# Optimization experiments

Hardware: AMD Instinct MI355X
Metric: run time of the kernel (lower is better)

## Reference

```python
import jax, jax.numpy as jnp
import numpy as np
from jax import lax


def leaky(x):
    return jax.nn.leaky_relu(x, 0.01)


def masked_softmax(vec, mask, eps=1e-6):
    # softmax over entries where mask>0; zero elsewhere (stable via masked max)
    mask = mask.astype(vec.dtype)
    mx = jnp.max(jnp.where(mask > 0, vec, -jnp.inf), axis=1, keepdims=True)
    mx = jnp.where(jnp.isfinite(mx), mx, 0.0)
    e = jnp.exp(vec - mx) * mask
    return e / (e.sum(axis=1, keepdims=True) + eps)


def gru_dir(x, w_ih, w_hh, b_ih, b_hh, reverse):
    # PyTorch GRU cell math, one direction. x: [T, in]
    gi_all = x @ w_ih.T + b_ih  # [T, 3*GH], input gates precomputed
    def step(h, gi):
        gh = h @ w_hh.T + b_hh
        i_r, i_z, i_n = jnp.split(gi, 3)
        h_r, h_z, h_n = jnp.split(gh, 3)
        r = jax.nn.sigmoid(i_r + h_r)
        z = jax.nn.sigmoid(i_z + h_z)
        n = jnp.tanh(i_n + r * h_n)
        h2 = (1.0 - z) * n + z * h
        return h2, h2
    h0 = jnp.zeros((w_hh.shape[1],), x.dtype)
    _, ys = lax.scan(step, h0, gi_all, reverse=reverse)
    return ys  # [T, GH]


def setup_inputs():
    key = jax.random.key(0)
    ks = jax.random.split(key, 30)
    W, P, R, H = 128, 4096, 8192, 1024
    GH = H // 2
    s = 0.05
    def nrm(k, shp, sc):
        return jax.random.normal(k, shp, jnp.float32) * sc
    return {
        "word_feat": nrm(ks[0], (W, H), 1.0),
        "phrase_feat": nrm(ks[1], (P, H), 1.0),
        "rel_feat": nrm(ks[2], (R, H), 1.0),
        "w_ih_f": nrm(ks[3], (3 * GH, H), s), "w_hh_f": nrm(ks[4], (3 * GH, GH), s),
        "b_ih_f": nrm(ks[5], (3 * GH,), s), "b_hh_f": nrm(ks[6], (3 * GH,), s),
        "w_ih_b": nrm(ks[7], (3 * GH, H), s), "w_hh_b": nrm(ks[8], (3 * GH, GH), s),
        "b_ih_b": nrm(ks[9], (3 * GH,), s), "b_hh_b": nrm(ks[10], (3 * GH,), s),
        "w2p_w_W": nrm(ks[11], (H, H), s), "w2p_w_b": nrm(ks[12], (H,), s),
        "w2p_p_W": nrm(ks[13], (H, H), s), "w2p_p_b": nrm(ks[14], (H,), s),
        "w2p_t_W": nrm(ks[15], (H, H), s), "w2p_t_b": nrm(ks[16], (H,), s),
        "rel_W": nrm(ks[17], (H, 3 * H), s), "rel_b": nrm(ks[18], (H,), s),
        "att1_W": nrm(ks[19], (H, 4 * H), s), "att1_b": nrm(ks[20], (H,), s),
        "att2_W": nrm(ks[21], (1, H), s), "att2_b": nrm(ks[22], (1,), s),
        "r2p_t_W": nrm(ks[23], (H, H), s), "r2p_t_b": nrm(ks[24], (H,), s),
        "rel_conn_mat": jax.random.randint(ks[25], (2, R), 0, P),
        "word_to_graph_conn": jax.random.randint(ks[26], (P, W), 0, 2),
    }


def reference(word_feat, phrase_feat, rel_feat, w_ih_f, w_hh_f, b_ih_f, b_hh_f,
              w_ih_b, w_hh_b, b_ih_b, b_hh_b, w2p_w_W, w2p_w_b, w2p_p_W, w2p_p_b,
              w2p_t_W, w2p_t_b, rel_W, rel_b, att1_W, att1_b, att2_W, att2_b,
              r2p_t_W, r2p_t_b, rel_conn_mat, word_to_graph_conn):
    H = word_feat.shape[1]
    # bidirectional GRU over the word sequence
    lf = jnp.concatenate([
        gru_dir(word_feat, w_ih_f, w_hh_f, b_ih_f, b_hh_f, False),
        gru_dir(word_feat, w_ih_b, w_hh_b, b_ih_b, b_hh_b, True),
    ], axis=1)  # [T, H]
    ctx = jnp.concatenate([lf[0], lf[-1]])[None, :]  # [1, 2H]
    # word -> phrase attention
    a = (leaky(phrase_feat @ w2p_p_W.T + w2p_p_b)
         @ leaky(word_feat @ w2p_w_W.T + w2p_w_b).T) / jnp.sqrt(jnp.float32(H))
    a = masked_softmax(a, word_to_graph_conn)
    upd = phrase_feat + (a @ word_feat) @ w2p_t_W.T + w2p_t_b  # [P, H]
    # phrase -> rel
    sub, obj = rel_conn_mat[0], rel_conn_mat[1]
    Rn = sub.shape[0]
    Pn = upd.shape[0]
    urel = jnp.concatenate([upd[sub], upd[obj], rel_feat], 1) @ rel_W.T + rel_b  # [R, H]
    # rel -> phrase with sparse connectivity (each rel touches subject+object)
    ar = jnp.arange(Rn)
    mask = jnp.zeros((Pn, Rn), upd.dtype).at[sub, ar].set(1.0).at[obj, ar].set(1.0)
    ix = jnp.concatenate([sub, obj])
    iy = jnp.concatenate([ar, ar])
    fuse = jnp.concatenate(
        [upd[ix], urel[iy], jnp.broadcast_to(ctx, (ix.shape[0], ctx.shape[1]))], 1)  # [2R, 4H]
    s = (leaky(fuse @ att1_W.T + att1_b) @ att2_W.T + att2_b)[:, 0]
    att = jnp.zeros((Pn, Rn), upd.dtype).at[ix, iy].set(s)
    att = masked_softmax(att, mask)
    out_phrase = upd + (att @ urel) @ r2p_t_W.T + r2p_t_b
    return (word_feat, out_phrase, urel)
```

## Files before the change

kernel.cpp:

```cpp
#include <hip/hip_runtime.h>

#define DEV __device__ __forceinline__

typedef short s16x8 __attribute__((ext_vector_type(8)));
typedef float f32x4 __attribute__((ext_vector_type(4)));
typedef __fp16 fp16x8 __attribute__((ext_vector_type(8)));
typedef unsigned short u16;
typedef unsigned long long u64;

constexpr int Wn = 128;
constexpr int Pn = 4096;
constexpr int Rn = 8192;
constexpr int Hn = 1024;

DEV float b2f(u16 u) { union { unsigned i; float f; } x; x.i = (unsigned)u << 16; return x.f; }
DEV u16 f2b(float f) {
  union { float f; unsigned i; } x; x.f = f;
  unsigned r = x.i + 0x7FFF + ((x.i >> 16) & 1);
  return (u16)(r >> 16);
}
DEV u16 f2h(float x) { __fp16 h = (__fp16)x; u16 r; __builtin_memcpy(&r, &h, 2); return r; }
DEV float leaky(float x) { return x >= 0.f ? x : 0.01f * x; }

DEV void load_lds16(const void* g, void* l) {
  __builtin_amdgcn_global_load_lds(
      (const __attribute__((address_space(1))) void*)g,
      (__attribute__((address_space(3))) void*)l, 16, 0, 0);
}

DEV float wred_sum(float v) {
  #pragma unroll
  for (int m = 1; m < 64; m <<= 1) v += __shfl_xor(v, m, 64);
  return v;
}
DEV float wred_max(float v) {
  #pragma unroll
  for (int m = 1; m < 64; m <<= 1) v = fmaxf(v, __shfl_xor(v, m, 64));
  return v;
}

__global__ __launch_bounds__(256) void k_cvt(
    const float* __restrict__ src, int sld, u16* __restrict__ dst)
{
  int g = blockIdx.x * 256 + threadIdx.x;
  int row = g >> 7, c = (g & 127) * 8;
  const float* s = src + (size_t)row * sld + c;
  float4 a = *(const float4*)s;
  float4 b = *(const float4*)(s + 4);
  ushort4 lo = {f2b(a.x), f2b(a.y), f2b(a.z), f2b(a.w)};
  ushort4 hi = {f2b(b.x), f2b(b.y), f2b(b.z), f2b(b.w)};
  *(ushort4*)(dst + (size_t)row * 1024 + c) = lo;
  *(ushort4*)(dst + (size_t)row * 1024 + c + 4) = hi;
}

template<bool OUTF32, bool ACT, bool BIAS, bool RES, bool DUAL>
DEV void gemm_tile(char* sm,
    const u16* __restrict__ A, int lda, const u16* __restrict__ B, int ldb,
    void* Cp, int ldc, const float* __restrict__ bias,
    const float* res, int ldr, u16* C16, float alpha, int K, int m0, int n0)
{
  char* As = sm;
  char* Bs = sm + 16384;
  const int tid = threadIdx.x;
  const int lane = tid & 63, w = tid >> 6;
  const int wr = (w >> 1) * 64, wc = (w & 1) * 64;
  const int r_lo = lane & 15, kq = lane >> 4;

  __syncthreads();

  f32x4 acc[4][4];
  #pragma unroll
  for (int i = 0; i < 4; ++i)
    #pragma unroll
    for (int j = 0; j < 4; ++j) acc[i][j] = (f32x4){0.f, 0.f, 0.f, 0.f};

  for (int kt = 0; kt < K; kt += 64) {
    if (kt) __syncthreads();
    #pragma unroll
    for (int i = 0; i < 4; ++i) {
      int f = i * 4096 + tid * 16;
      int row = f >> 7, colb = f & 127;
      int scol = colb ^ ((row & 7) << 4);
      load_lds16((const char*)(A + (size_t)(m0 + row) * lda + kt) + scol,
                 As + i * 4096 + w * 1024);
    }
    #pragma unroll
    for (int i = 0; i < 4; ++i) {
      int f = i * 4096 + tid * 16;
      int row = f >> 7, colb = f & 127;
      int scol = colb ^ ((row & 7) << 4);
      load_lds16((const char*)(B + (size_t)(n0 + row) * ldb + kt) + scol,
                 Bs + i * 4096 + w * 1024);
    }
    __syncthreads();
    #pragma unroll
    for (int ks = 0; ks < 2; ++ks) {
      s16x8 af[4], bfr[4];
      const int kb = ks * 64 + kq * 16;
      #pragma unroll
      for (int mi = 0; mi < 4; ++mi) {
        int row = wr + mi * 16 + r_lo;
        af[mi] = *(const s16x8*)(As + row * 128 + (kb ^ ((row & 7) << 4)));
      }
      #pragma unroll
      for (int ni = 0; ni < 4; ++ni) {
        int row = wc + ni * 16 + r_lo;
        bfr[ni] = *(const s16x8*)(Bs + row * 128 + (kb ^ ((row & 7) << 4)));
      }
      #pragma unroll
      for (int mi = 0; mi < 4; ++mi)
        #pragma unroll
        for (int ni = 0; ni < 4; ++ni)
          acc[mi][ni] = __builtin_amdgcn_mfma_f32_16x16x32_bf16(af[mi], bfr[ni], acc[mi][ni], 0, 0, 0);
    }
  }
  #pragma unroll
  for (int mi = 0; mi < 4; ++mi)
    #pragma unroll
    for (int ni = 0; ni < 4; ++ni)
      #pragma unroll
      for (int j = 0; j < 4; ++j) {
        int r = m0 + wr + mi * 16 + kq * 4 + j;
        int c = n0 + wc + ni * 16 + r_lo;
        float v = acc[mi][ni][j] * alpha;
        if (BIAS) v += bias[c];
        if (RES)  v += res[(size_t)r * ldr + c];
        if (ACT)  v = leaky(v);
        if (OUTF32) ((float*)Cp)[(size_t)r * ldc + c] = v;
        else        ((u16*)Cp)[(size_t)r * ldc + c] = f2b(v);
        if (DUAL)   C16[(size_t)r * ldc + c] = f2b(v);
      }
}

template<bool OUTF32, bool ACT, bool BIAS, bool RES, bool DUAL>
__global__ __launch_bounds__(256) void k_gemm_bt(
    const u16* __restrict__ A, int lda, const u16* __restrict__ B, int ldb,
    void* Cp, int ldc, const float* __restrict__ bias,
    const float* res, int ldr, u16* C16, float alpha, int K)
{
  __shared__ __align__(16) char sm[32768];
  gemm_tile<OUTF32, ACT, BIAS, RES, DUAL>(sm, A, lda, B, ldb, Cp, ldc, bias,
      res, ldr, C16, alpha, K, blockIdx.y * 128, blockIdx.x * 128);
}

__global__ __launch_bounds__(256) void k_rf3(
    const u16* __restrict__ G, const u16* __restrict__ relU,
    const u16* __restrict__ W3s, const float* __restrict__ rel_b,
    float* __restrict__ out_urel)
{
  __shared__ __align__(16) char sm[32768];
  int half = blockIdx.y >> 5;
  gemm_tile<true, false, true, false, false>(sm,
      half ? relU : G, Hn, W3s, Hn,
      out_urel + (size_t)half * 4096 * Hn, Hn, rel_b, nullptr, 0, nullptr,
      1.f, Hn, (blockIdx.y & 31) * 128, blockIdx.x * 128);
}

__global__ __launch_bounds__(256) void k_gemm_rel(
    const u16* __restrict__ upd16, const int* __restrict__ rcm,
    const u16* __restrict__ W1, const u16* __restrict__ W2,
    float* __restrict__ out_urel)
{
  __shared__ __align__(16) char sm[32768];
  __shared__ int ridx[2][128];
  char* As = sm;
  char* Bs = sm + 16384;
  const int tid = threadIdx.x;
  const int lane = tid & 63, w = tid >> 6;
  const int hh = blockIdx.y >> 5;
  const int m0 = (blockIdx.y & 31) * 128, n0 = blockIdx.x * 128;
  const int wr = (w >> 1) * 64, wc = (w & 1) * 64;
  const int r_lo = lane & 15, kq = lane >> 4;
  const int* sub = rcm + hh * 4096;
  const int* obj = rcm + Rn + hh * 4096;
  float* C = out_urel + (size_t)hh * 4096 * Hn;

  if (tid < 128) ridx[0][tid] = sub[m0 + tid];
  else ridx[1][tid - 128] = obj[m0 + tid - 128];
  __syncthreads();

  f32x4 acc[4][4];
  #pragma unroll
  for (int i = 0; i < 4; ++i)
    #pragma unroll
    for (int j = 0; j < 4; ++j) acc[i][j] = (f32x4){0.f, 0.f, 0.f, 0.f};

  for (int kt = 0; kt < 2048; kt += 64) {
    const int half = kt >> 10;
    const int kk = kt & 1023;
    const u16* Wm = half ? W2 : W1;
    __syncthreads();
    #pragma unroll
    for (int i = 0; i < 4; ++i) {
      int f = i * 4096 + tid * 16;
      int row = f >> 7, colb = f & 127;
      int scol = colb ^ ((row & 7) << 4);
      load_lds16((const char*)(upd16 + (size_t)ridx[half][row] * 1024 + kk) + scol,
                 As + i * 4096 + w * 1024);
    }
    #pragma unroll
    for (int i = 0; i < 4; ++i) {
      int f = i * 4096 + tid * 16;
      int row = f >> 7, colb = f & 127;
      int scol = colb ^ ((row & 7) << 4);
      load_lds16((const char*)(Wm + (size_t)(n0 + row) * 1024 + kk) + scol,
                 Bs + i * 4096 + w * 1024);
    }
    __syncthreads();
    #pragma unroll
    for (int ks = 0; ks < 2; ++ks) {
      s16x8 af[4], bfr[4];
      const int kb = ks * 64 + kq * 16;
      #pragma unroll
      for (int mi = 0; mi < 4; ++mi) {
        int row = wr + mi * 16 + r_lo;
        af[mi] = *(const s16x8*)(As + row * 128 + (kb ^ ((row & 7) << 4)));
      }
      #pragma unroll
      for (int ni = 0; ni < 4; ++ni) {
        int row = wc + ni * 16 + r_lo;
        bfr[ni] = *(const s16x8*)(Bs + row * 128 + (kb ^ ((row & 7) << 4)));
      }
      #pragma unroll
      for (int mi = 0; mi < 4; ++mi)
        #pragma unroll
        for (int ni = 0; ni < 4; ++ni)
          acc[mi][ni] = __builtin_amdgcn_mfma_f32_16x16x32_bf16(af[mi], bfr[ni], acc[mi][ni], 0, 0, 0);
    }
  }
  #pragma unroll
  for (int mi = 0; mi < 4; ++mi)
    #pragma unroll
    for (int ni = 0; ni < 4; ++ni)
      #pragma unroll
      for (int j = 0; j < 4; ++j) {
        int r = m0 + wr + mi * 16 + kq * 4 + j;
        int c = n0 + wc + ni * 16 + r_lo;
        C[(size_t)r * Hn + c] = acc[mi][ni][j] + C[(size_t)r * Hn + c];
      }
}

struct CvtTask { const float* src; u16* dst; int sld; int units; };
struct MKArgs {
  const float *w_hh_f, *w_hh_b, *b_hh_f, *b_hh_b;
  const float *word_feat, *w_ih_f, *w_ih_b, *b_ih_f, *b_ih_b;
  const int* rcm;
  float *gi_f, *gi_b;
  u16 *wf16, *wih16f, *wih16b;
  u64* X; int* cntX; int* pc; int* cnt2; int* offs; int* cursor;
  float* ctx;
  CvtTask t[11]; int nt;
};

__global__ __launch_bounds__(256) void k_mega(MKArgs a)
{
  __shared__ __align__(16) u16 wlds[96 * 512];
  __shared__ float bh[96];
  __shared__ float partg[4][96];
  __shared__ __align__(16) u16 hb[512];

  const int bid = blockIdx.x;
  const int tid = threadIdx.x;
  const int lane = tid & 63, wv = tid >> 6;
  const int NW = (int)gridDim.x - 32;

  if (bid >= 32) {
    const int bc = bid - 32, nb = NW;
    int bar = 0;
    auto wbarrier = [&]() {
      __syncthreads();
      if (tid == 0) {
        __hip_atomic_fetch_add(&a.pc[bar], 1, __ATOMIC_ACQ_REL, __HIP_MEMORY_SCOPE_AGENT);
        while (__hip_atomic_load(&a.pc[bar], __ATOMIC_ACQUIRE, __HIP_MEMORY_SCOPE_AGENT) < NW)
          __builtin_amdgcn_s_sleep(4);
      }
      __syncthreads();
      ++bar;
    };
    auto cvt_task = [&](const float* src, int sld, u16* dst, int units) {
      for (int u = bc * 256 + tid; u < units; u += nb * 256) {
        int row = u >> 7, c = (u & 127) * 8;
        const float* s = src + (size_t)row * sld + c;
        float4 va = *(const float4*)s;
        float4 vb = *(const float4*)(s + 4);
        ushort4 lo = {f2b(va.x), f2b(va.y), f2b(va.z), f2b(va.w)};
        ushort4 hi = {f2b(vb.x), f2b(vb.y), f2b(vb.z), f2b(vb.w)};
        *(ushort4*)(dst + (size_t)row * 1024 + c) = lo;
        *(ushort4*)(dst + (size_t)row * 1024 + c + 4) = hi;
      }
    };

    cvt_task(a.word_feat, Hn, a.wf16, Wn * 128);
    cvt_task(a.w_ih_f, Hn, a.wih16f, 1536 * 128);
    cvt_task(a.w_ih_b, Hn, a.wih16b, 1536 * 128);
    wbarrier();
    for (int u = bc; u < 24; u += nb) {
      const u16* Bm = u < 12 ? a.wih16f : a.wih16b;
      float* Cm = u < 12 ? a.gi_f : a.gi_b;
      const float* bm = u < 12 ? a.b_ih_f : a.b_ih_b;
      gemm_tile<true, false, true, false, false>((char*)wlds, a.wf16, Hn, Bm, Hn,
          Cm, 1536, bm, nullptr, 0, nullptr, 1.f, Hn, 0, (u % 12) * 128);
    }
    for (int u = bc * 256 + tid; u < 2 * Rn; u += nb * 256) {
      if (u < Rn && a.rcm[u] == a.rcm[Rn + u]) continue;
      atomicAdd(a.cnt2 + a.rcm[u], 1);
    }
    wbarrier();
    if (bc == 0) {
      int* part = (int*)wlds;
      int* pscan = part + 256;
      int loc[16]; int s = 0;
      #pragma unroll
      for (int i = 0; i < 16; ++i) { loc[i] = a.cnt2[tid * 16 + i]; s += loc[i]; }
      part[tid] = s; __syncthreads();
      if (tid == 0) { int acc = 0; for (int i = 0; i < 256; ++i) { pscan[i] = acc; acc += part[i]; } }
      __syncthreads();
      int base = pscan[tid];
      #pragma unroll
      for (int i = 0; i < 16; ++i) {
        a.offs[tid * 16 + i] = base; a.cursor[tid * 16 + i] = base; base += loc[i];
      }
      if (tid == 255) a.offs[Pn] = base;
    }
    for (int k = 0; k < a.nt; ++k)
      cvt_task(a.t[k].src, a.t[k].sld, a.t[k].dst, a.t[k].units);
    return;
  }

  const int dir = bid >> 4;
  const int b   = bid & 15;
  const float* w_hh = dir ? a.w_hh_b : a.w_hh_f;
  const float* b_hhp = dir ? a.b_hh_b : a.b_hh_f;
  const float* gi = dir ? a.gi_b : a.gi_f;
  u64* Xd = a.X + (size_t)dir * 128 * 128;
  int* cntD = a.cntX + dir * 128;

  for (int idx = tid; idx < 96 * 128; idx += 256) {
    int gl = idx >> 7;
    int kc = (idx & 127) << 2;
    int g  = 32 * b + (gl & 31) + ((gl >> 5) << 9);
    float4 wv4 = *(const float4*)(w_hh + (size_t)g * 512 + kc);
    u16 d4[4] = {f2h(wv4.x), f2h(wv4.y), f2h(wv4.z), f2h(wv4.w)};
    int byte = (kc * 2) ^ ((gl & 7) << 4);
    *(uint2*)((char*)wlds + gl * 1024 + byte) = *(uint2*)d4;
  }
  if (tid < 96) {
    int g = 32 * b + (tid & 31) + ((tid >> 5) << 9);
    bh[tid] = b_hhp[g];
  }
  for (int i = tid; i < 256; i += 256) ((unsigned*)hb)[i] = 0u;
  if (tid == 0) {
    while (__hip_atomic_load(&a.pc[1], __ATOMIC_ACQUIRE, __HIP_MEMORY_SCOPE_AGENT) < NW)
      __builtin_amdgcn_s_sleep(16);
  }
  __syncthreads();

  float hprev = 0.f;
  const int jg = 32 * b + tid;
  const int r_lo = lane & 15, kq = lane >> 4;
  const fp16x8 zf = {0, 0, 0, 0, 0, 0, 0, 0};

  for (int sidx = 0; sidx < 128; ++sidx) {
    const int t = dir ? (127 - sidx) : sidx;

    float gir = 0.f, giz = 0.f, gin = 0.f;
    if (tid < 32) {
      gir = gi[t * 1536 + jg];
      giz = gi[t * 1536 + 512 + jg];
      gin = gi[t * 1536 + 1024 + jg];
    }

    f32x4 acc6[6];
    #pragma unroll
    for (int gt = 0; gt < 6; ++gt) acc6[gt] = (f32x4){0.f, 0.f, 0.f, 0.f};
    #pragma unroll
    for (int k2 = 0; k2 < 4; ++k2) {
      int kt = (wv << 2) + k2;
      fp16x8 bf = (r_lo == 0) ? *(const fp16x8*)(hb + kt * 32 + kq * 8) : zf;
      #pragma unroll
      for (int gt = 0; gt < 6; ++gt) {
        int gl = gt * 16 + r_lo;
        int byte = (kt * 64 + kq * 16) ^ ((gl & 7) << 4);
        fp16x8 af = *(const fp16x8*)((const char*)wlds + gl * 1024 + byte);
        acc6[gt] = __builtin_amdgcn_mfma_f32_16x16x32_f16(af, bf, acc6[gt], 0, 0, 0);
      }
    }
    if (r_lo == 0) {
      #pragma unroll
      for (int gt = 0; gt < 6; ++gt)
        #pragma unroll
        for (int j = 0; j < 4; ++j)
          partg[wv][gt * 16 + kq * 4 + j] = acc6[gt][j];
    }
    __syncthreads();

    if (wv == 0) {
      float h2v = 0.f;
      if (lane < 32) {
        int j = lane;
        float ghr = partg[0][j] + partg[1][j] + partg[2][j] + partg[3][j] + bh[j];
        float ghz = partg[0][j + 32] + partg[1][j + 32] + partg[2][j + 32] + partg[3][j + 32] + bh[j + 32];
        float ghn = partg[0][j + 64] + partg[1][j + 64] + partg[2][j + 64] + partg[3][j + 64] + bh[j + 64];
        float rr = 1.f / (1.f + __expf(-(gir + ghr)));
        float zz = 1.f / (1.f + __expf(-(giz + ghz)));
        float nn = tanhf(gin + rr * ghn);
        h2v = (1.f - zz) * nn + zz * hprev;
        hprev = h2v;
        if (sidx == 0)   a.ctx[(dir ? 1536 : 0)    + jg] = h2v;
        if (sidx == 127) a.ctx[(dir ? 512  : 1024) + jg] = h2v;
      }
      if (sidx < 127) {
        int l4 = (lane & 7) * 4;
        float p0 = __shfl(h2v, l4 + 0, 64);
        float p1 = __shfl(h2v, l4 + 1, 64);
        float p2 = __shfl(h2v, l4 + 2, 64);
        float p3 = __shfl(h2v, l4 + 3, 64);
        if (lane < 8) {
          u64 pk = (u64)f2h(p0) | ((u64)f2h(p1) << 16) |
                   ((u64)f2h(p2) << 32) | ((u64)f2h(p3) << 48);
          __hip_atomic_store(&Xd[(size_t)sidx * 128 + b * 8 + lane], pk,
                             __ATOMIC_RELAXED, __HIP_MEMORY_SCOPE_AGENT);
        }
        if (lane == 0)
          __hip_atomic_fetch_add(&cntD[sidx], 1, __ATOMIC_RELEASE,
                                 __HIP_MEMORY_SCOPE_AGENT);
        while (__hip_atomic_load(&cntD[sidx], __ATOMIC_ACQUIRE,
                                 __HIP_MEMORY_SCOPE_AGENT) < 16)
          __builtin_amdgcn_s_sleep(1);
        const u64* src = Xd + (size_t)sidx * 128;
        u64 w0 = __hip_atomic_load(&src[2 * lane],     __ATOMIC_RELAXED, __HIP_MEMORY_SCOPE_AGENT);
        u64 w1 = __hip_atomic_load(&src[2 * lane + 1], __ATOMIC_RELAXED, __HIP_MEMORY_SCOPE_AGENT);
        *(u64*)(hb + lane * 8)     = w0;
        *(u64*)(hb + lane * 8 + 4) = w1;
      }
    }
    __syncthreads();
  }
}

__global__ __launch_bounds__(256) void k_softmax1(
    const float* __restrict__ scores, const int* __restrict__ conn, u16* __restrict__ attw)
{
  int p = blockIdx.x * 4 + (threadIdx.x >> 6);
  int lane = threadIdx.x & 63;
  float v0 = scores[(size_t)p * 128 + lane];
  float v1 = scores[(size_t)p * 128 + 64 + lane];
  int m0 = conn[(size_t)p * 128 + lane];
  int m1 = conn[(size_t)p * 128 + 64 + lane];
  float x0 = m0 > 0 ? v0 : -INFINITY;
  float x1 = m1 > 0 ? v1 : -INFINITY;
  float mx = wred_max(fmaxf(x0, x1));
  if (!(mx > -INFINITY)) mx = 0.f;
  float e0 = m0 > 0 ? __expf(v0 - mx) : 0.f;
  float e1 = m1 > 0 ? __expf(v1 - mx) : 0.f;
  float s = wred_sum(e0 + e1);
  float inv = 1.f / (s + 1e-6f);
  attw[(size_t)p * 128 + lane] = f2b(e0 * inv);
  attw[(size_t)p * 128 + 64 + lane] = f2b(e1 * inv);
}

__global__ __launch_bounds__(256) void k_transpose(const u16* __restrict__ in, u16* __restrict__ out)
{
  int idx = blockIdx.x * 256 + threadIdx.x;
  int r = idx >> 10, c = idx & 1023;
  out[c * 128 + r] = in[idx];
}

__global__ __launch_bounds__(256) void k_cvec(const float* __restrict__ att1W,
    const float* __restrict__ att1b, const float* __restrict__ ctx, float* __restrict__ cvec)
{
  int i = blockIdx.x * 4 + (threadIdx.x >> 6);
  int lane = threadIdx.x & 63;
  const float* wrow = att1W + (size_t)i * 4096 + 2048 + lane * 32;
  const float* cp = ctx + lane * 32;
  float acc = 0.f;
  #pragma unroll
  for (int k = 0; k < 32; ++k) acc += wrow[k] * cp[k];
  acc = wred_sum(acc);
  if (lane == 0) cvec[i] = acc + att1b[i];
}

__global__ __launch_bounds__(256) void k_edge_s(const int* __restrict__ rcm,
    const u16* __restrict__ U1, const u16* __restrict__ V1, const float* __restrict__ cvec,
    const float* __restrict__ att2w, const float* __restrict__ att2b,
    float* __restrict__ sval)
{
  int idx = blockIdx.x * 4 + (threadIdx.x >> 6);
  int lane = threadIdx.x & 63;
  int rL = idx < Rn ? idx : idx - Rn;
  int p = rcm[idx];
  const u16* u = U1 + (size_t)p * Hn + lane * 16;
  const u16* v = V1 + (size_t)rL * Hn + lane * 16;
  const float* aw = att2w + lane * 16;
  const float* cv = cvec + lane * 16;
  float acc = 0.f;
  #pragma unroll
  for (int i = 0; i < 16; ++i) {
    float x = b2f(u[i]) + b2f(v[i]) + cv[i];
    acc += aw[i] * leaky(x);
  }
  acc = wred_sum(acc);
  if (lane == 0) sval[idx] = acc + att2b[0];
}

__global__ __launch_bounds__(256) void k_fill(const int* __restrict__ rcm,
    const float* __restrict__ sval, int* __restrict__ cursor,
    int* __restrict__ er, float* __restrict__ es)
{
  int e = blockIdx.x * 256 + threadIdx.x;
  if (e < Rn && rcm[e] == rcm[Rn + e]) return;
  int slot = atomicAdd(cursor + rcm[e], 1);
  er[slot] = e & (Rn - 1);
  es[slot] = sval[e];
}

__global__ __launch_bounds__(256) void k_att_apply(const int* __restrict__ offs,
    const int* __restrict__ er, const float* __restrict__ es,
    const float* __restrict__ urel, u16* __restrict__ pacc)
{
  int p = blockIdx.x;
  int tid = threadIdx.x;
  int beg = offs[p], end = offs[p + 1];
  float mx = -INFINITY;
  for (int i = beg; i < end; ++i) mx = fmaxf(mx, es[i]);
  float den = 1e-6f;
  for (int i = beg; i < end; ++i) den += __expf(es[i] - mx);
  float inv = 1.f / den;
  float a0 = 0.f, a1 = 0.f, a2 = 0.f, a3 = 0.f;
  int c0 = tid * 4;
  for (int i = beg; i < end; ++i) {
    float wgt = __expf(es[i] - mx) * inv;
    float4 q = *(const float4*)(urel + (size_t)er[i] * Hn + c0);
    a0 += wgt * q.x; a1 += wgt * q.y; a2 += wgt * q.z; a3 += wgt * q.w;
  }
  ushort4 ov; ov.x = f2b(a0); ov.y = f2b(a1); ov.z = f2b(a2); ov.w = f2b(a3);
  *(ushort4*)(pacc + (size_t)p * Hn + c0) = ov;
}

extern "C" void kernel_launch(void* const* d_in, const int* in_sizes, int n_in,
                              void* d_out, int out_size, void* d_ws, size_t ws_size,
                              hipStream_t stream)
{
  const float* word_feat   = (const float*)d_in[0];
  const float* phrase_feat = (const float*)d_in[1];
  const float* rel_feat    = (const float*)d_in[2];
  const float* w_ih_f = (const float*)d_in[3];
  const float* w_hh_f = (const float*)d_in[4];
  const float* b_ih_f = (const float*)d_in[5];
  const float* b_hh_f = (const float*)d_in[6];
  const float* w_ih_b = (const float*)d_in[7];
  const float* w_hh_b = (const float*)d_in[8];
  const float* b_ih_b = (const float*)d_in[9];
  const float* b_hh_b = (const float*)d_in[10];
  const float* w2p_w_W = (const float*)d_in[11];
  const float* w2p_w_b = (const float*)d_in[12];
  const float* w2p_p_W = (const float*)d_in[13];
  const float* w2p_p_b = (const float*)d_in[14];
  const float* w2p_t_W = (const float*)d_in[15];
  const float* w2p_t_b = (const float*)d_in[16];
  const float* rel_W   = (const float*)d_in[17];
  const float* rel_b   = (const float*)d_in[18];
  const float* att1_W  = (const float*)d_in[19];
  const float* att1_b  = (const float*)d_in[20];
  const float* att2_W  = (const float*)d_in[21];
  const float* att2_b  = (const float*)d_in[22];
  const float* r2p_t_W = (const float*)d_in[23];
  const float* r2p_t_b = (const float*)d_in[24];
  const int* rcm  = (const int*)d_in[25];
  const int* conn = (const int*)d_in[26];

  float* out_word = (float*)d_out;
  float* out_phr  = out_word + (size_t)Wn * Hn;
  float* out_urel = out_phr + (size_t)Pn * Hn;

  char* ws = (char*)d_ws;
  size_t off = 0;
  auto alloc = [&](size_t bytes) -> char* {
    char* pptr = ws + off; off += (bytes + 255) & ~(size_t)255; return pptr;
  };
  int*   cnt2   = (int*)alloc(Pn * 4);
  int*   pc     = (int*)alloc(64 * 4);
  int*   cntX   = (int*)alloc(256 * 4);
  u64*   X      = (u64*)alloc(2 * 128 * 128 * 8);
  size_t zlen   = (size_t)((char*)(X + 2 * 128 * 128) - (char*)cnt2);
  float* ctx    = (float*)alloc(2048 * 4);
  float* cvec   = (float*)alloc(1024 * 4);
  int*   cursor = (int*)alloc(Pn * 4);
  int*   offs   = (int*)alloc((Pn + 1) * 4);
  int*   er     = (int*)alloc(2 * Rn * 4);
  float* es     = (float*)alloc(2 * Rn * 4);
  float* sval   = (float*)alloc(2 * Rn * 4);
  float* gi_f   = (float*)alloc(128 * 1536 * 4);
  float* gi_b   = (float*)alloc(128 * 1536 * 4);
  u16*   wf16   = (u16*)alloc((size_t)Wn * Hn * 2);
  u16*   wl     = (u16*)alloc((size_t)Wn * Hn * 2);
  u16*   upd16  = (u16*)alloc((size_t)Pn * Hn * 2);
  char*  RA     = alloc(16777216);
  u16*   W1s    = (u16*)RA;
  u16*   W2s    = (u16*)(RA + 2097152);
  u16*   W3s    = (u16*)(RA + 4194304);
  u16*   G      = (u16*)(RA + 6291456);
  u16*   V1f    = (u16*)RA;
  u16*   A1p16  = (u16*)alloc(2097152);
  u16*   A1r16  = (u16*)alloc(2097152);
  u16*   U1     = (u16*)alloc((size_t)Pn * Hn * 2);
  u16*   relU16 = U1;
  char*  CBr    = alloc(4194304);
  u16*   CB     = (u16*)CBr;
  u16*   r2pW16 = (u16*)CBr;
  u16*   pacc   = upd16;

  char* phrB = (char*)out_phr;
  u16*   wih16f = (u16*)phrB;
  u16*   wih16b = (u16*)(phrB + 3145728);
  float* scores = (float*)(phrB + 6291456);
  char* urlB = (char*)out_urel;
  u16*   pf16   = (u16*)urlB;
  u16*   w2pw16 = (u16*)(urlB + 8388608);
  u16*   w2pp16 = (u16*)(urlB + 10485760);
  u16*   w2pt16 = (u16*)(urlB + 12582912);
  u16*   pl     = (u16*)(urlB + 14680064);
  u16*   aw     = (u16*)(urlB + 23068672);
  u16*   attw   = (u16*)(urlB + 31457280);
  u16*   wfT    = (u16*)(urlB + 32505856);

  (void)hipMemsetAsync(cnt2, 0, zlen, stream);

  dim3 blk(256);

  MKArgs A;
  A.w_hh_f = w_hh_f; A.w_hh_b = w_hh_b; A.b_hh_f = b_hh_f; A.b_hh_b = b_hh_b;
  A.word_feat = word_feat; A.w_ih_f = w_ih_f; A.w_ih_b = w_ih_b;
  A.b_ih_f = b_ih_f; A.b_ih_b = b_ih_b; A.rcm = rcm;
  A.gi_f = gi_f; A.gi_b = gi_b;
  A.wf16 = wf16; A.wih16f = wih16f; A.wih16b = wih16b;
  A.X = X; A.cntX = cntX; A.pc = pc; A.cnt2 = cnt2;
  A.offs = offs; A.cursor = cursor; A.ctx = ctx;
  A.t[0]  = {phrase_feat,    pf16,   Hn,     Pn * 128};
  A.t[1]  = {w2p_w_W,        w2pw16, Hn,     1024 * 128};
  A.t[2]  = {w2p_p_W,        w2pp16, Hn,     1024 * 128};
  A.t[3]  = {w2p_t_W,        w2pt16, Hn,     1024 * 128};
  A.t[4]  = {rel_W,          W1s,    3 * Hn, 1024 * 128};
  A.t[5]  = {rel_W + Hn,     W2s,    3 * Hn, 1024 * 128};
  A.t[6]  = {rel_W + 2 * Hn, W3s,    3 * Hn, 1024 * 128};
  A.t[7]  = {att1_W,         A1p16,  4 * Hn, 1024 * 128};
  A.t[8]  = {att1_W + Hn,    A1r16,  4 * Hn, 1024 * 128};
  A.t[9]  = {rel_feat,       G,      Hn,     4096 * 128};
  A.t[10] = {rel_feat + (size_t)4096 * Hn, relU16, Hn, 4096 * 128};
  A.nt = 11;
  k_mega<<<256, blk, 0, stream>>>(A);
  k_cvec<<<256, blk, 0, stream>>>(att1_W, att1_b, ctx, cvec);

  k_gemm_bt<false, true, true, false, false><<<dim3(8, 1), blk, 0, stream>>>(
      wf16, Hn, w2pw16, Hn, wl, Hn, w2p_w_b, nullptr, 0, nullptr, 1.f, Hn);
  k_gemm_bt<false, true, true, false, false><<<dim3(8, 32), blk, 0, stream>>>(
      pf16, Hn, w2pp16, Hn, pl, Hn, w2p_p_b, nullptr, 0, nullptr, 1.f, Hn);
  k_gemm_bt<true, false, false, false, false><<<dim3(1, 32), blk, 0, stream>>>(
      pl, Hn, wl, Hn, scores, Wn, nullptr, nullptr, 0, nullptr, 0.03125f, Hn);
  k_softmax1<<<Pn / 4, blk, 0, stream>>>(scores, conn, attw);
  k_transpose<<<(Wn * Hn) / 256, blk, 0, stream>>>(wf16, wfT);
  k_gemm_bt<false, false, false, false, false><<<dim3(8, 32), blk, 0, stream>>>(
      attw, Wn, wfT, Wn, aw, Hn, nullptr, nullptr, 0, nullptr, 1.f, Wn);
  k_gemm_bt<true, false, true, true, true><<<dim3(8, 32), blk, 0, stream>>>(
      aw, Hn, w2pt16, Hn, out_phr, Hn, w2p_t_b, phrase_feat, Hn, upd16, 1.f, Hn);

  k_rf3<<<dim3(8, 64), blk, 0, stream>>>(G, relU16, W3s, rel_b, out_urel);
  k_gemm_rel<<<dim3(8, 64), blk, 0, stream>>>(upd16, rcm, W1s, W2s, out_urel);

  k_gemm_bt<false, false, false, false, false><<<dim3(8, 32), blk, 0, stream>>>(
      upd16, Hn, A1p16, Hn, U1, Hn, nullptr, nullptr, 0, nullptr, 1.f, Hn);
  for (int cb = 0; cb < Rn; cb += 2048) {
    k_cvt<<<1024, blk, 0, stream>>>(out_urel + (size_t)cb * Hn, Hn, CB);
    k_gemm_bt<false, false, false, false, false><<<dim3(8, 16), blk, 0, stream>>>(
        CB, Hn, A1r16, Hn, V1f + (size_t)cb * Hn, Hn, nullptr, nullptr, 0,
        nullptr, 1.f, Hn);
  }
  k_cvt<<<512, blk, 0, stream>>>(r2p_t_W, Hn, r2pW16);

  k_edge_s<<<(2 * Rn) / 4, blk, 0, stream>>>(rcm, U1, V1f, cvec, att2_W, att2_b, sval);
  k_fill<<<(2 * Rn) / 256, blk, 0, stream>>>(rcm, sval, cursor, er, es);
  k_att_apply<<<Pn, blk, 0, stream>>>(offs, er, es, out_urel, pacc);
  k_gemm_bt<true, false, true, true, false><<<dim3(8, 32), blk, 0, stream>>>(
      pacc, Hn, r2pW16, Hn, out_phr, Hn, r2p_t_b, out_phr, Hn, nullptr, 1.f, Hn);

  (void)hipMemcpyAsync(out_word, word_feat, (size_t)Wn * Hn * 4,
                       hipMemcpyDeviceToDevice, stream);
}
```

Baseline: 798.1 us.

## Overlap word-phrase attention with GRU in megakernel; fuse fp32 cast into GEMM

Moves the word-to-phrase attention chain (two projections, scores GEMM, masked softmax, transpose, aw GEMM, update GEMM) into the worker blocks of the persistent megakernel. These stages are separated by grid barriers and run while the 32 GRU blocks execute their recurrence, which removes several launches and hides the work behind the serial scan. The chunked fp32-to-bf16 conversion of urel followed by a GEMM is replaced by a single GEMM that converts fp32 A tiles while loading them into shared memory. The GRU hidden-state exchange now tags each packed word with a step number instead of using a separate counter atomic, so readers poll the data directly. In exchange, the attention GEMMs run on fewer blocks (the 224 workers), and the fused conversion adds VALU work to the GEMM's load path.

```diff
diff --git a/kernel.cpp b/kernel.cpp
--- a/kernel.cpp
+++ b/kernel.cpp
@@ -37,20 +37,6 @@
   #pragma unroll
   for (int m = 1; m < 64; m <<= 1) v = fmaxf(v, __shfl_xor(v, m, 64));
   return v;
-}
-
-__global__ __launch_bounds__(256) void k_cvt(
-    const float* __restrict__ src, int sld, u16* __restrict__ dst)
-{
-  int g = blockIdx.x * 256 + threadIdx.x;
-  int row = g >> 7, c = (g & 127) * 8;
-  const float* s = src + (size_t)row * sld + c;
-  float4 a = *(const float4*)s;
-  float4 b = *(const float4*)(s + 4);
-  ushort4 lo = {f2b(a.x), f2b(a.y), f2b(a.z), f2b(a.w)};
-  ushort4 hi = {f2b(b.x), f2b(b.y), f2b(b.z), f2b(b.w)};
-  *(ushort4*)(dst + (size_t)row * 1024 + c) = lo;
-  *(ushort4*)(dst + (size_t)row * 1024 + c + 4) = hi;
 }
 
 template<bool OUTF32, bool ACT, bool BIAS, bool RES, bool DUAL>
@@ -141,6 +127,81 @@
   __shared__ __align__(16) char sm[32768];
   gemm_tile<OUTF32, ACT, BIAS, RES, DUAL>(sm, A, lda, B, ldb, Cp, ldc, bias,
       res, ldr, C16, alpha, K, blockIdx.y * 128, blockIdx.x * 128);
+}
+
+__global__ __launch_bounds__(256) void k_gemm_af32(
+    const float* __restrict__ A, int lda, const u16* __restrict__ B, int ldb,
+    u16* __restrict__ C, int ldc, int K)
+{
+  __shared__ __align__(16) char sm[32768];
+  char* As = sm;
+  char* Bs = sm + 16384;
+  const int tid = threadIdx.x;
+  const int lane = tid & 63, w = tid >> 6;
+  const int m0 = blockIdx.y * 128, n0 = blockIdx.x * 128;
+  const int wr = (w >> 1) * 64, wc = (w & 1) * 64;
+  const int r_lo = lane & 15, kq = lane >> 4;
+
+  f32x4 acc[4][4];
+  #pragma unroll
+  for (int i = 0; i < 4; ++i)
+    #pragma unroll
+    for (int j = 0; j < 4; ++j) acc[i][j] = (f32x4){0.f, 0.f, 0.f, 0.f};
+
+  for (int kt = 0; kt < K; kt += 64) {
+    if (kt) __syncthreads();
+    #pragma unroll
+    for (int i = 0; i < 4; ++i) {
+      int e = i * 2048 + tid * 8;
+      int row = e >> 6, col = e & 63;
+      const float* s = A + (size_t)(m0 + row) * lda + kt + col;
+      float4 a4 = *(const float4*)s;
+      float4 b4 = *(const float4*)(s + 4);
+      u16 d8[8] = {f2b(a4.x), f2b(a4.y), f2b(a4.z), f2b(a4.w),
+                   f2b(b4.x), f2b(b4.y), f2b(b4.z), f2b(b4.w)};
+      int byte = (col * 2) ^ ((row & 7) << 4);
+      *(uint4*)(As + row * 128 + byte) = *(uint4*)d8;
+    }
+    #pragma unroll
+    for (int i = 0; i < 4; ++i) {
+      int f = i * 4096 + tid * 16;
+      int row = f >> 7, colb = f & 127;
+      int scol = colb ^ ((row & 7) << 4);
+      load_lds16((const char*)(B + (size_t)(n0 + row) * ldb + kt) + scol,
+                 Bs + i * 4096 + w * 1024);
+    }
+    __syncthreads();
+    #pragma unroll
+    for (int ks = 0; ks < 2; ++ks) {
+      s16x8 af[4], bfr[4];
+      const int kb = ks * 64 + kq * 16;
+      #pragma unroll
+      for (int mi = 0; mi < 4; ++mi) {
+        int row = wr + mi * 16 + r_lo;
+        af[mi] = *(const s16x8*)(As + row * 128 + (kb ^ ((row & 7) << 4)));
+      }
+      #pragma unroll
+      for (int ni = 0; ni < 4; ++ni) {
+        int row = wc + ni * 16 + r_lo;
+        bfr[ni] = *(const s16x8*)(Bs + row * 128 + (kb ^ ((row & 7) << 4)));
+      }
+      #pragma unroll
+      for (int mi = 0; mi < 4; ++mi)
+        #pragma unroll
+        for (int ni = 0; ni < 4; ++ni)
+          acc[mi][ni] = __builtin_amdgcn_mfma_f32_16x16x32_bf16(af[mi], bfr[ni], acc[mi][ni], 0, 0, 0);
+    }
+  }
+  #pragma unroll
+  for (int mi = 0; mi < 4; ++mi)
+    #pragma unroll
+    for (int ni = 0; ni < 4; ++ni)
+      #pragma unroll
+      for (int j = 0; j < 4; ++j) {
+        int r = m0 + wr + mi * 16 + kq * 4 + j;
+        int c = n0 + wc + ni * 16 + r_lo;
+        C[(size_t)r * ldc + c] = f2b(acc[mi][ni][j]);
+      }
 }
 
 __global__ __launch_bounds__(256) void k_rf3(
@@ -244,12 +305,13 @@
 struct MKArgs {
   const float *w_hh_f, *w_hh_b, *b_hh_f, *b_hh_b;
   const float *word_feat, *w_ih_f, *w_ih_b, *b_ih_f, *b_ih_b;
-  const int* rcm;
-  float *gi_f, *gi_b;
-  u16 *wf16, *wih16f, *wih16b;
-  u64* X; int* cntX; int* pc; int* cnt2; int* offs; int* cursor;
-  float* ctx;
-  CvtTask t[11]; int nt;
+  const float *phrase_feat, *w2p_w_b, *w2p_p_b, *w2p_t_b;
+  const int *rcm, *conn;
+  float *gi_f, *gi_b, *scores, *out_phr, *ctx;
+  u16 *wf16, *wih16f, *wih16b, *wl;
+  u16 *pf16, *w2pw16, *w2pp16, *w2pt16, *pl, *attw, *wfT, *aw, *upd16;
+  u64* X; int* pc; int* cnt2; int* offs; int* cursor;
+  CvtTask t[12]; int nt;
 };
 
 __global__ __launch_bounds__(256) void k_mega(MKArgs a)
@@ -321,9 +383,63 @@
         a.offs[tid * 16 + i] = base; a.cursor[tid * 16 + i] = base; base += loc[i];
       }
       if (tid == 255) a.offs[Pn] = base;
+      __syncthreads();
     }
     for (int k = 0; k < a.nt; ++k)
       cvt_task(a.t[k].src, a.t[k].sld, a.t[k].dst, a.t[k].units);
+    wbarrier();
+    for (int u = bc; u < 264; u += nb) {
+      if (u < 8)
+        gemm_tile<false, true, true, false, false>((char*)wlds, a.wf16, Hn,
+            a.w2pw16, Hn, a.wl, Hn, a.w2p_w_b, nullptr, 0, nullptr, 1.f, Hn,
+            0, u * 128);
+      else {
+        int t2 = u - 8;
+        gemm_tile<false, true, true, false, false>((char*)wlds, a.pf16, Hn,
+            a.w2pp16, Hn, a.pl, Hn, a.w2p_p_b, nullptr, 0, nullptr, 1.f, Hn,
+            (t2 >> 3) * 128, (t2 & 7) * 128);
+      }
+    }
+    wbarrier();
+    for (int u = bc; u < 544; u += nb) {
+      if (u < 32)
+        gemm_tile<true, false, false, false, false>((char*)wlds, a.pl, Hn,
+            a.wl, Hn, a.scores, Wn, nullptr, nullptr, 0, nullptr, 0.03125f, Hn,
+            u * 128, 0);
+      else {
+        int idx = (u - 32) * 256 + tid;
+        int r = idx >> 10, c = idx & 1023;
+        a.wfT[c * 128 + r] = a.wf16[idx];
+      }
+    }
+    wbarrier();
+    for (int u = bc; u < 1024; u += nb) {
+      int p = u * 4 + wv;
+      float v0 = a.scores[(size_t)p * 128 + lane];
+      float v1 = a.scores[(size_t)p * 128 + 64 + lane];
+      int m0 = a.conn[(size_t)p * 128 + lane];
+      int m1 = a.conn[(size_t)p * 128 + 64 + lane];
+      float x0 = m0 > 0 ? v0 : -INFINITY;
+      float x1 = m1 > 0 ? v1 : -INFINITY;
+      float mx = wred_max(fmaxf(x0, x1));
+      if (!(mx > -INFINITY)) mx = 0.f;
+      float e0 = m0 > 0 ? __expf(v0 - mx) : 0.f;
+      float e1 = m1 > 0 ? __expf(v1 - mx) : 0.f;
+      float s = wred_sum(e0 + e1);
+      float inv = 1.f / (s + 1e-6f);
+      a.attw[(size_t)p * 128 + lane] = f2b(e0 * inv);
+      a.attw[(size_t)p * 128 + 64 + lane] = f2b(e1 * inv);
+    }
+    wbarrier();
+    for (int u = bc; u < 256; u += nb)
+      gemm_tile<false, false, false, false, false>((char*)wlds, a.attw, Wn,
+          a.wfT, Wn, a.aw, Hn, nullptr, nullptr, 0, nullptr, 1.f, Wn,
+          (u >> 3) * 128, (u & 7) * 128);
+    wbarrier();
+    for (int u = bc; u < 256; u += nb)
+      gemm_tile<true, false, true, true, true>((char*)wlds, a.aw, Hn,
+          a.w2pt16, Hn, a.out_phr, Hn, a.w2p_t_b, a.phrase_feat, Hn, a.upd16,
+          1.f, Hn, (u >> 3) * 128, (u & 7) * 128);
     return;
   }
 
@@ -332,8 +448,7 @@
   const float* w_hh = dir ? a.w_hh_b : a.w_hh_f;
   const float* b_hhp = dir ? a.b_hh_b : a.b_hh_f;
   const float* gi = dir ? a.gi_b : a.gi_f;
-  u64* Xd = a.X + (size_t)dir * 128 * 128;
-  int* cntD = a.cntX + dir * 128;
+  u64* Xd = a.X + (size_t)dir * 128 * 256;
 
   for (int idx = tid; idx < 96 * 128; idx += 256) {
     int gl = idx >> 7;
@@ -410,60 +525,38 @@
         if (sidx == 127) a.ctx[(dir ? 512  : 1024) + jg] = h2v;
       }
       if (sidx < 127) {
-        int l4 = (lane & 7) * 4;
-        float p0 = __shfl(h2v, l4 + 0, 64);
-        float p1 = __shfl(h2v, l4 + 1, 64);
-        float p2 = __shfl(h2v, l4 + 2, 64);
-        float p3 = __shfl(h2v, l4 + 3, 64);
-        if (lane < 8) {
-          u64 pk = (u64)f2h(p0) | ((u64)f2h(p1) << 16) |
-                   ((u64)f2h(p2) << 32) | ((u64)f2h(p3) << 48);
-          __hip_atomic_store(&Xd[(size_t)sidx * 128 + b * 8 + lane], pk,
+        float q0 = __shfl(h2v, (lane & 15) * 2, 64);
+        float q1 = __shfl(h2v, (lane & 15) * 2 + 1, 64);
+        if (lane < 16) {
+          u64 pk = (u64)f2h(q0) | ((u64)f2h(q1) << 16) |
+                   ((u64)(unsigned)(sidx + 1) << 32);
+          __hip_atomic_store(&Xd[(size_t)sidx * 256 + b * 16 + lane], pk,
                              __ATOMIC_RELAXED, __HIP_MEMORY_SCOPE_AGENT);
         }
-        if (lane == 0)
-          __hip_atomic_fetch_add(&cntD[sidx], 1, __ATOMIC_RELEASE,
-                                 __HIP_MEMORY_SCOPE_AGENT);
-        while (__hip_atomic_load(&cntD[sidx], __ATOMIC_ACQUIRE,
-                                 __HIP_MEMORY_SCOPE_AGENT) < 16)
-          __builtin_amdgcn_s_sleep(1);
-        const u64* src = Xd + (size_t)sidx * 128;
-        u64 w0 = __hip_atomic_load(&src[2 * lane],     __ATOMIC_RELAXED, __HIP_MEMORY_SCOPE_AGENT);
-        u64 w1 = __hip_atomic_load(&src[2 * lane + 1], __ATOMIC_RELAXED, __HIP_MEMORY_SCOPE_AGENT);
-        *(u64*)(hb + lane * 8)     = w0;
-        *(u64*)(hb + lane * 8 + 4) = w1;
+        const u64* src = Xd + (size_t)sidx * 256;
+        const unsigned want = (unsigned)(sidx + 1);
+        const int base = lane * 4;
+        u64 v[4];
+        unsigned done = 0;
+        while (done != 0xFu) {
+          #pragma unroll
+          for (int i = 0; i < 4; ++i)
+            if (!(done & (1u << i)))
+              v[i] = __hip_atomic_load(&src[base + i], __ATOMIC_RELAXED,
+                                       __HIP_MEMORY_SCOPE_AGENT);
+          #pragma unroll
+          for (int i = 0; i < 4; ++i)
+            if (!(done & (1u << i)) && (unsigned)(v[i] >> 32) == want)
+              done |= 1u << i;
+          if (done != 0xFu) __builtin_amdgcn_s_sleep(1);
+        }
+        #pragma unroll
+        for (int i = 0; i < 4; ++i)
+          ((unsigned*)hb)[base + i] = (unsigned)v[i];
       }
     }
     __syncthreads();
   }
-}
-
-__global__ __launch_bounds__(256) void k_softmax1(
-    const float* __restrict__ scores, const int* __restrict__ conn, u16* __restrict__ attw)
-{
-  int p = blockIdx.x * 4 + (threadIdx.x >> 6);
-  int lane = threadIdx.x & 63;
-  float v0 = scores[(size_t)p * 128 + lane];
-  float v1 = scores[(size_t)p * 128 + 64 + lane];
-  int m0 = conn[(size_t)p * 128 + lane];
-  int m1 = conn[(size_t)p * 128 + 64 + lane];
-  float x0 = m0 > 0 ? v0 : -INFINITY;
-  float x1 = m1 > 0 ? v1 : -INFINITY;
-  float mx = wred_max(fmaxf(x0, x1));
-  if (!(mx > -INFINITY)) mx = 0.f;
-  float e0 = m0 > 0 ? __expf(v0 - mx) : 0.f;
-  float e1 = m1 > 0 ? __expf(v1 - mx) : 0.f;
-  float s = wred_sum(e0 + e1);
-  float inv = 1.f / (s + 1e-6f);
-  attw[(size_t)p * 128 + lane] = f2b(e0 * inv);
-  attw[(size_t)p * 128 + 64 + lane] = f2b(e1 * inv);
-}
-
-__global__ __launch_bounds__(256) void k_transpose(const u16* __restrict__ in, u16* __restrict__ out)
-{
-  int idx = blockIdx.x * 256 + threadIdx.x;
-  int r = idx >> 10, c = idx & 1023;
-  out[c * 128 + r] = in[idx];
 }
 
 __global__ __launch_bounds__(256) void k_cvec(const float* __restrict__ att1W,
@@ -580,9 +673,8 @@
   };
   int*   cnt2   = (int*)alloc(Pn * 4);
   int*   pc     = (int*)alloc(64 * 4);
-  int*   cntX   = (int*)alloc(256 * 4);
-  u64*   X      = (u64*)alloc(2 * 128 * 128 * 8);
-  size_t zlen   = (size_t)((char*)(X + 2 * 128 * 128) - (char*)cnt2);
+  u64*   X      = (u64*)alloc(2 * 128 * 256 * 8);
+  size_t zlen   = (size_t)((char*)(X + 2 * 128 * 256) - (char*)cnt2);
   float* ctx    = (float*)alloc(2048 * 4);
   float* cvec   = (float*)alloc(1024 * 4);
   int*   cursor = (int*)alloc(Pn * 4);
@@ -605,9 +697,7 @@
   u16*   A1r16  = (u16*)alloc(2097152);
   u16*   U1     = (u16*)alloc((size_t)Pn * Hn * 2);
   u16*   relU16 = U1;
-  char*  CBr    = alloc(4194304);
-  u16*   CB     = (u16*)CBr;
-  u16*   r2pW16 = (u16*)CBr;
+  u16*   r2pW16 = (u16*)alloc(2097152);
   u16*   pacc   = upd16;
 
   char* phrB = (char*)out_phr;
@@ -631,11 +721,14 @@
   MKArgs A;
   A.w_hh_f = w_hh_f; A.w_hh_b = w_hh_b; A.b_hh_f = b_hh_f; A.b_hh_b = b_hh_b;
   A.word_feat = word_feat; A.w_ih_f = w_ih_f; A.w_ih_b = w_ih_b;
-  A.b_ih_f = b_ih_f; A.b_ih_b = b_ih_b; A.rcm = rcm;
-  A.gi_f = gi_f; A.gi_b = gi_b;
-  A.wf16 = wf16; A.wih16f = wih16f; A.wih16b = wih16b;
-  A.X = X; A.cntX = cntX; A.pc = pc; A.cnt2 = cnt2;
-  A.offs = offs; A.cursor = cursor; A.ctx = ctx;
+  A.b_ih_f = b_ih_f; A.b_ih_b = b_ih_b;
+  A.phrase_feat = phrase_feat; A.w2p_w_b = w2p_w_b; A.w2p_p_b = w2p_p_b;
+  A.w2p_t_b = w2p_t_b; A.rcm = rcm; A.conn = conn;
+  A.gi_f = gi_f; A.gi_b = gi_b; A.scores = scores; A.out_phr = out_phr; A.ctx = ctx;
+  A.wf16 = wf16; A.wih16f = wih16f; A.wih16b = wih16b; A.wl = wl;
+  A.pf16 = pf16; A.w2pw16 = w2pw16; A.w2pp16 = w2pp16; A.w2pt16 = w2pt16;
+  A.pl = pl; A.attw = attw; A.wfT = wfT; A.aw = aw; A.upd16 = upd16;
+  A.X = X; A.pc = pc; A.cnt2 = cnt2; A.offs = offs; A.cursor = cursor;
   A.t[0]  = {phrase_feat,    pf16,   Hn,     Pn * 128};
   A.t[1]  = {w2p_w_W,        w2pw16, Hn,     1024 * 128};
   A.t[2]  = {w2p_p_W,        w2pp16, Hn,     1024 * 128};
@@ -645,37 +738,20 @@
   A.t[6]  = {rel_W + 2 * Hn, W3s,    3 * Hn, 1024 * 128};
   A.t[7]  = {att1_W,         A1p16,  4 * Hn, 1024 * 128};
   A.t[8]  = {att1_W + Hn,    A1r16,  4 * Hn, 1024 * 128};
-  A.t[9]  = {rel_feat,       G,      Hn,     4096 * 128};
-  A.t[10] = {rel_feat + (size_t)4096 * Hn, relU16, Hn, 4096 * 128};
-  A.nt = 11;
+  A.t[9]  = {r2p_t_W,        r2pW16, Hn,     1024 * 128};
+  A.t[10] = {rel_feat,       G,      Hn,     4096 * 128};
+  A.t[11] = {rel_feat + (size_t)4096 * Hn, relU16, Hn, 4096 * 128};
+  A.nt = 12;
   k_mega<<<256, blk, 0, stream>>>(A);
   k_cvec<<<256, blk, 0, stream>>>(att1_W, att1_b, ctx, cvec);
 
-  k_gemm_bt<false, true, true, false, false><<<dim3(8, 1), blk, 0, stream>>>(
-      wf16, Hn, w2pw16, Hn, wl, Hn, w2p_w_b, nullptr, 0, nullptr, 1.f, Hn);
-  k_gemm_bt<false, true, true, false, false><<<dim3(8, 32), blk, 0, stream>>>(
-      pf16, Hn, w2pp16, Hn, pl, Hn, w2p_p_b, nullptr, 0, nullptr, 1.f, Hn);
-  k_gemm_bt<true, false, false, false, false><<<dim3(1, 32), blk, 0, stream>>>(
-      pl, Hn, wl, Hn, scores, Wn, nullptr, nullptr, 0, nullptr, 0.03125f, Hn);
-  k_softmax1<<<Pn / 4, blk, 0, stream>>>(scores, conn, attw);
-  k_transpose<<<(Wn * Hn) / 256, blk, 0, stream>>>(wf16, wfT);
-  k_gemm_bt<false, false, false, false, false><<<dim3(8, 32), blk, 0, stream>>>(
-      attw, Wn, wfT, Wn, aw, Hn, nullptr, nullptr, 0, nullptr, 1.f, Wn);
-  k_gemm_bt<true, false, true, true, true><<<dim3(8, 32), blk, 0, stream>>>(
-      aw, Hn, w2pt16, Hn, out_phr, Hn, w2p_t_b, phrase_feat, Hn, upd16, 1.f, Hn);
-
   k_rf3<<<dim3(8, 64), blk, 0, stream>>>(G, relU16, W3s, rel_b, out_urel);
   k_gemm_rel<<<dim3(8, 64), blk, 0, stream>>>(upd16, rcm, W1s, W2s, out_urel);
 
   k_gemm_bt<false, false, false, false, false><<<dim3(8, 32), blk, 0, stream>>>(
       upd16, Hn, A1p16, Hn, U1, Hn, nullptr, nullptr, 0, nullptr, 1.f, Hn);
-  for (int cb = 0; cb < Rn; cb += 2048) {
-    k_cvt<<<1024, blk, 0, stream>>>(out_urel + (size_t)cb * Hn, Hn, CB);
-    k_gemm_bt<false, false, false, false, false><<<dim3(8, 16), blk, 0, stream>>>(
-        CB, Hn, A1r16, Hn, V1f + (size_t)cb * Hn, Hn, nullptr, nullptr, 0,
-        nullptr, 1.f, Hn);
-  }
-  k_cvt<<<512, blk, 0, stream>>>(r2p_t_W, Hn, r2pW16);
+  k_gemm_af32<<<dim3(8, 64), blk, 0, stream>>>(
+      out_urel, Hn, A1r16, Hn, V1f, Hn, Hn);
 
   k_edge_s<<<(2 * Rn) / 4, blk, 0, stream>>>(rcm, U1, V1f, cvec, att2_W, att2_b, sval);
   k_fill<<<(2 * Rn) / 256, blk, 0, stream>>>(rcm, sval, cursor, er, es);
```

Measured after the change: 736.9 us. -7.7%, faster.
